# Optimization experiments

Measured on AMD Instinct MI355X. Metric: run time of the kernel, lower is better.

The kernel has to match this reference:

```python
import jax, jax.numpy as jnp
import numpy as np

N = 8192
DIM = 128


def setup_inputs() -> dict:
    key = jax.random.key(0)
    k1, k2 = jax.random.split(key)
    mapping = jax.random.normal(k1, (N, DIM), dtype=jnp.float32)
    # Cost matrix of the finite metric: symmetric, strictly positive off-diagonal,
    # zero diagonal (the module adds eye to the denominator to handle the diagonal).
    Draw = jax.random.uniform(k2, (N, N), dtype=jnp.float32) * 2.0 + 0.1
    D = 0.5 * (Draw + Draw.T)
    D = D * (1.0 - jnp.eye(N, dtype=jnp.float32))
    return {"mapping": mapping, "D": D}


def reference(mapping, D):
    # Pairwise Euclidean distances via GEMM formulation (||a||^2 - 2ab + ||b||^2)
    # instead of materializing the O(N^2 * dim) broadcast difference.
    n = D.shape[0]
    sq = jnp.sum(mapping * mapping, axis=-1)               # [N]
    gram = mapping @ mapping.T                             # [N, N]
    d2 = sq[:, None] + sq[None, :] - 2.0 * gram            # [N, N]
    d2 = jnp.maximum(d2, 0.0)
    # safe sqrt (exact 0 on the diagonal, matching torch.norm forward)
    pos = d2 > 0
    d = jnp.sqrt(jnp.where(pos, d2, 1.0)) * pos
    ratio = jnp.abs(d - D) / (D + jnp.eye(n, dtype=D.dtype))
    return jnp.sum(ratio) / (n * n - n)
```

## Files before the change

kernel.cpp:

```cpp
#include <hip/hip_runtime.h>
#include <math.h>

#define NN 8192
#define DIM 128
#define NBLK 1024

typedef short bf16x8 __attribute__((ext_vector_type(8)));
typedef float f32x4 __attribute__((ext_vector_type(4)));

__device__ inline unsigned short f2bf(float x) {
    unsigned u = __float_as_uint(x);
    unsigned r = u + 0x7FFFu + ((u >> 16) & 1u);
    return (unsigned short)(r >> 16);
}
__device__ inline float bf2f(unsigned short h) {
    return __uint_as_float(((unsigned)h) << 16);
}

__global__ void pack_kernel(const float* __restrict__ m, unsigned short* __restrict__ buf2) {
    const int t = threadIdx.x, l = t & 63;
    const int W = blockIdx.x * 4 + (t >> 6);
    const int g = W >> 2, kq = W & 3;
    const int row = g * 16 + (l & 15);
    const int k0 = kq * 32 + (l >> 4) * 8;
    const float* src = m + (size_t)row * DIM + k0;
    float4 v0 = *reinterpret_cast<const float4*>(src);
    float4 v1 = *reinterpret_cast<const float4*>(src + 4);
    float f[8] = {v0.x, v0.y, v0.z, v0.w, v1.x, v1.y, v1.z, v1.w};
    union { ushort4 u4[2]; unsigned short us[8]; } o;
#pragma unroll
    for (int q = 0; q < 8; ++q) o.us[q] = f2bf(f[q]);
    unsigned short* dst = buf2 + (size_t)W * 512 + l * 8;
    *reinterpret_cast<ushort4*>(dst) = o.u4[0];
    *reinterpret_cast<ushort4*>(dst + 4) = o.u4[1];
}

__global__ void sq_kernel(const float* __restrict__ mapping, float* __restrict__ sq) {
    int i = blockIdx.x * blockDim.x + threadIdx.x;
    if (i < NN) {
        const float4* row = reinterpret_cast<const float4*>(mapping + (size_t)i * DIM);
        float s = 0.f;
#pragma unroll
        for (int q = 0; q < DIM / 4; ++q) {
            float4 v = row[q];
            s += v.x * v.x + v.y * v.y + v.z * v.z + v.w * v.w;
        }
        sq[i] = s;
    }
}

__global__ __launch_bounds__(512, 6) void dist_kernel(const unsigned short* __restrict__ buf2,
                                                      const float* __restrict__ D,
                                                      const float* __restrict__ sq,
                                                      float* __restrict__ partials) {
    __shared__ __align__(16) char dtile[4][64 * 144];
    __shared__ float wred[8];

    const int t = threadIdx.x, l = t & 63, w = t >> 6;
    const int b = blockIdx.x;
    const int q = b >> 3, p = b & 7;
    const int cj0 = q + p;
    float psum = 0.f;

    if (cj0 < 128) {
        const int nt = ((127 - cj0) >> 3) + 1;
        const int l15 = l & 15, hi = l >> 4;
        const int colq = hi * 4;
        const int strip = w & 3;
        const int i_row = q * 64 + strip * 16 + l15;
        const int ldsoff = (strip * 16 + l15) * 144 + hi * 8;

        if (w < 4) {
            bf16x8 af[4];
#pragma unroll
            for (int kq = 0; kq < 4; ++kq)
                af[kq] = *(const bf16x8*)(buf2 + (size_t)((q * 4 + strip) * 4 + kq) * 512 + l * 8);
            const float sa = sq[i_row];

            for (int tt = 0; tt < nt; ++tt) {
                const int cj = cj0 + tt * 8;
                char* slot = &dtile[tt & 3][0];
#pragma unroll
                for (int s = 0; s < 4; ++s) {
                    bf16x8 bfr[4];
#pragma unroll
                    for (int kq = 0; kq < 4; ++kq)
                        bfr[kq] = *(const bf16x8*)(buf2 + (size_t)((cj * 4 + s) * 4 + kq) * 512 + l * 8);
                    f32x4 sb = *(const f32x4*)(sq + cj * 64 + s * 16 + colq);
                    f32x4 acc = {};
#pragma unroll
                    for (int kq = 0; kq < 4; ++kq)
                        acc = __builtin_amdgcn_mfma_f32_16x16x32_bf16(bfr[kq], af[kq], acc, 0, 0, 0);
                    ushort4 o;
                    unsigned short* op = (unsigned short*)&o;
#pragma unroll
                    for (int r = 0; r < 4; ++r) {
                        float d2 = fmaf(-2.f, acc[r], sa + sb[r]);
                        op[r] = f2bf(sqrtf(fmaxf(d2, 0.f)));
                    }
                    *reinterpret_cast<ushort4*>(slot + ldsoff + s * 32) = o;
                }
                if ((tt & 1) == 1 || tt == nt - 1) {
                    asm volatile("s_waitcnt lgkmcnt(0)" ::: "memory");
                    __builtin_amdgcn_sched_barrier(0);
                    __builtin_amdgcn_s_barrier();
                }
            }
        } else {
            const float* Drow = D + (size_t)i_row * NN;

            auto consume = [&](int tile, const f32x4(&dc)[4]) {
                const int cj = cj0 + tile * 8;
                const char* slot = &dtile[tile & 3][0];
                if (cj != q) {
#pragma unroll
                    for (int s = 0; s < 4; ++s) {
                        ushort4 o = *reinterpret_cast<const ushort4*>(slot + ldsoff + s * 32);
                        const unsigned short* op = (const unsigned short*)&o;
#pragma unroll
                        for (int r = 0; r < 4; ++r) {
                            float Dv = dc[s][r];
                            psum += __fdividef(fabsf(bf2f(op[r]) - Dv), Dv);
                        }
                    }
                } else {
#pragma unroll
                    for (int s = 0; s < 4; ++s) {
                        ushort4 o = *reinterpret_cast<const ushort4*>(slot + ldsoff + s * 32);
                        const unsigned short* op = (const unsigned short*)&o;
#pragma unroll
                        for (int r = 0; r < 4; ++r) {
                            const int j = cj * 64 + s * 16 + colq + r;
                            if (j > i_row) {
                                float Dv = dc[s][r];
                                psum += __fdividef(fabsf(bf2f(op[r]) - Dv), Dv);
                            }
                        }
                    }
                }
            };

            f32x4 dA[4], dB[4];
#pragma unroll
            for (int s = 0; s < 4; ++s)
                dA[s] = *(const f32x4*)(Drow + cj0 * 64 + s * 16 + colq);

            bool cur_a = true;
            for (int tt = 0; tt < nt; ++tt) {
                if ((tt & 1) == 0) __builtin_amdgcn_s_barrier();
                const int ncj = cj0 + (tt + 1) * 8;
                if (cur_a) {
                    if (tt + 1 < nt) {
#pragma unroll
                        for (int s = 0; s < 4; ++s)
                            dB[s] = *(const f32x4*)(Drow + ncj * 64 + s * 16 + colq);
                    }
                    consume(tt, dA);
                } else {
                    if (tt + 1 < nt) {
#pragma unroll
                        for (int s = 0; s < 4; ++s)
                            dA[s] = *(const f32x4*)(Drow + ncj * 64 + s * 16 + colq);
                    }
                    consume(tt, dB);
                }
                cur_a = !cur_a;
            }
        }
    }

    for (int off = 32; off > 0; off >>= 1) psum += __shfl_down(psum, off, 64);
    __syncthreads();
    if (l == 0) wred[w] = psum;
    __syncthreads();
    if (t == 0) {
        float s = 0.f;
#pragma unroll
        for (int k = 0; k < 8; ++k) s += wred[k];
        partials[b] = 2.f * s;
    }
}

__global__ void reduce_kernel(const float* __restrict__ partials, float* __restrict__ out) {
    __shared__ double sm[256];
    const int t = threadIdx.x;
    double s = 0.0;
    for (int i = t; i < NBLK; i += 256) s += (double)partials[i];
    sm[t] = s;
    __syncthreads();
    for (int off = 128; off > 0; off >>= 1) {
        if (t < off) sm[t] += sm[t + off];
        __syncthreads();
    }
    if (t == 0) out[0] = (float)(sm[0] / ((double)NN * (double)NN - (double)NN));
}

extern "C" void kernel_launch(void* const* d_in, const int* in_sizes, int n_in,
                              void* d_out, int out_size, void* d_ws, size_t ws_size,
                              hipStream_t stream) {
    const float* mapping = (const float*)d_in[0];
    const float* D       = (const float*)d_in[1];
    float* out = (float*)d_out;

    unsigned short* buf2 = (unsigned short*)d_ws;
    float* sq            = (float*)(buf2 + NN * DIM);
    float* partials      = sq + NN;

    pack_kernel<<<512, 256, 0, stream>>>(mapping, buf2);
    sq_kernel<<<NN / 256, 256, 0, stream>>>(mapping, sq);
    dist_kernel<<<NBLK, 512, 0, stream>>>(buf2, D, sq, partials);
    reduce_kernel<<<1, 256, 0, stream>>>(partials, out);
}
```

Before: 68.14 us.

## Stage B operand tiles into LDS via direct global-to-LDS loads with double buffering

```diff
diff --git a/kernel.cpp b/kernel.cpp
--- a/kernel.cpp
+++ b/kernel.cpp
@@ -7,6 +7,11 @@
 
 typedef short bf16x8 __attribute__((ext_vector_type(8)));
 typedef float f32x4 __attribute__((ext_vector_type(4)));
+
+__device__ inline void gload_lds16(const void* g, void* l) {
+    __builtin_amdgcn_global_load_lds((const __attribute__((address_space(1))) void*)g,
+                                     (__attribute__((address_space(3))) void*)l, 16, 0, 0);
+}
 
 __device__ inline unsigned short f2bf(float x) {
     unsigned u = __float_as_uint(x);
@@ -53,7 +58,8 @@
                                                       const float* __restrict__ D,
                                                       const float* __restrict__ sq,
                                                       float* __restrict__ partials) {
-    __shared__ __align__(16) char dtile[4][64 * 144];
+    __shared__ __align__(16) char Bbuf[2][16384];
+    __shared__ __align__(16) char dtile[2][64 * 144];
     __shared__ float wred[8];
 
     const int t = threadIdx.x, l = t & 63, w = t >> 6;
@@ -77,16 +83,35 @@
                 af[kq] = *(const bf16x8*)(buf2 + (size_t)((q * 4 + strip) * 4 + kq) * 512 + l * 8);
             const float sa = sq[i_row];
 
+            f32x4 csb[4], nsb[4];
+#pragma unroll
+            for (int s = 0; s < 4; ++s)
+                csb[s] = *(const f32x4*)(sq + cj0 * 64 + s * 16 + colq);
+#pragma unroll
+            for (int kq = 0; kq < 4; ++kq)
+                gload_lds16(buf2 + (size_t)((cj0 * 4 + strip) * 4 + kq) * 512 + l * 8,
+                            (void*)&Bbuf[0][(strip * 4 + kq) * 1024]);
+            asm volatile("s_waitcnt vmcnt(0)" ::: "memory");
+            __builtin_amdgcn_s_barrier();
+
             for (int tt = 0; tt < nt; ++tt) {
-                const int cj = cj0 + tt * 8;
-                char* slot = &dtile[tt & 3][0];
+                const int slot = tt & 1;
+                if (tt + 1 < nt) {
+                    const int ncj = cj0 + (tt + 1) * 8;
+#pragma unroll
+                    for (int s = 0; s < 4; ++s)
+                        nsb[s] = *(const f32x4*)(sq + ncj * 64 + s * 16 + colq);
+#pragma unroll
+                    for (int kq = 0; kq < 4; ++kq)
+                        gload_lds16(buf2 + (size_t)((ncj * 4 + strip) * 4 + kq) * 512 + l * 8,
+                                    (void*)&Bbuf[slot ^ 1][(strip * 4 + kq) * 1024]);
+                }
 #pragma unroll
                 for (int s = 0; s < 4; ++s) {
                     bf16x8 bfr[4];
 #pragma unroll
                     for (int kq = 0; kq < 4; ++kq)
-                        bfr[kq] = *(const bf16x8*)(buf2 + (size_t)((cj * 4 + s) * 4 + kq) * 512 + l * 8);
-                    f32x4 sb = *(const f32x4*)(sq + cj * 64 + s * 16 + colq);
+                        bfr[kq] = *(const bf16x8*)&Bbuf[slot][(s * 4 + kq) * 1024 + l * 16];
                     f32x4 acc = {};
 #pragma unroll
                     for (int kq = 0; kq < 4; ++kq)
@@ -95,15 +120,17 @@
                     unsigned short* op = (unsigned short*)&o;
 #pragma unroll
                     for (int r = 0; r < 4; ++r) {
-                        float d2 = fmaf(-2.f, acc[r], sa + sb[r]);
+                        float d2 = fmaf(-2.f, acc[r], sa + csb[s][r]);
                         op[r] = f2bf(sqrtf(fmaxf(d2, 0.f)));
                     }
-                    *reinterpret_cast<ushort4*>(slot + ldsoff + s * 32) = o;
-                }
-                if ((tt & 1) == 1 || tt == nt - 1) {
-                    asm volatile("s_waitcnt lgkmcnt(0)" ::: "memory");
-                    __builtin_amdgcn_sched_barrier(0);
-                    __builtin_amdgcn_s_barrier();
+                    *reinterpret_cast<ushort4*>(&dtile[slot][0] + ldsoff + s * 32) = o;
+                }
+                asm volatile("s_waitcnt vmcnt(0) lgkmcnt(0)" ::: "memory");
+                __builtin_amdgcn_sched_barrier(0);
+                __builtin_amdgcn_s_barrier();
+                if (tt + 1 < nt) {
+#pragma unroll
+                    for (int s = 0; s < 4; ++s) csb[s] = nsb[s];
                 }
             }
         } else {
@@ -111,7 +138,7 @@
 
             auto consume = [&](int tile, const f32x4(&dc)[4]) {
                 const int cj = cj0 + tile * 8;
-                const char* slot = &dtile[tile & 3][0];
+                const char* slot = &dtile[tile & 1][0];
                 if (cj != q) {
 #pragma unroll
                     for (int s = 0; s < 4; ++s) {
@@ -144,26 +171,25 @@
 #pragma unroll
             for (int s = 0; s < 4; ++s)
                 dA[s] = *(const f32x4*)(Drow + cj0 * 64 + s * 16 + colq);
+            __builtin_amdgcn_s_barrier();
 
             bool cur_a = true;
             for (int tt = 0; tt < nt; ++tt) {
-                if ((tt & 1) == 0) __builtin_amdgcn_s_barrier();
-                const int ncj = cj0 + (tt + 1) * 8;
-                if (cur_a) {
-                    if (tt + 1 < nt) {
+                if (tt + 1 < nt) {
+                    const int ncj = cj0 + (tt + 1) * 8;
+                    if (cur_a) {
 #pragma unroll
                         for (int s = 0; s < 4; ++s)
                             dB[s] = *(const f32x4*)(Drow + ncj * 64 + s * 16 + colq);
-                    }
-                    consume(tt, dA);
-                } else {
-                    if (tt + 1 < nt) {
+                    } else {
 #pragma unroll
                         for (int s = 0; s < 4; ++s)
                             dA[s] = *(const f32x4*)(Drow + ncj * 64 + s * 16 + colq);
                     }
-                    consume(tt, dB);
-                }
+                }
+                __builtin_amdgcn_s_barrier();
+                if (cur_a) consume(tt, dA);
+                else       consume(tt, dB);
                 cur_a = !cur_a;
             }
         }
```

Result: faster. 65.94 us (-3.2%).
